# Performance work log

Measured on AMD Instinct MI355X. Metric: run time of the kernel, lower is better.

## Reference

```python
import jax, jax.numpy as jnp
import numpy as np

C_IMG = 16
GRID = 128
NV = 100000
NE = 1600000
CH = (32, 64, 64)
SCALE = 0.1
STEPS = 1
SLOPE = 0.3  # LeakyReLU default in module


def setup_inputs() -> dict:
    key = jax.random.key(0)
    ks = jax.random.split(key, 20)
    image_features = jax.random.normal(ks[0], (C_IMG, GRID, GRID, GRID), jnp.float32)
    # vertices live in voxel coordinates of the feature grid
    vertices = jax.random.uniform(ks[1], (NV, 3), jnp.float32) * (GRID - 1)
    edge_src = jax.random.randint(ks[2], (NE,), 0, NV, jnp.int32)
    edge_dst = jax.random.randint(ks[3], (NE,), 0, NV, jnp.int32)
    dims = [C_IMG + 3] + list(CH) + [3]  # +3 normalized positions
    inp = {"image_features": image_features, "vertices": vertices,
           "edge_src": edge_src, "edge_dst": edge_dst}
    ki = 4
    for i in range(len(dims) - 1):
        fan_in = dims[i]
        s = 1.0 / np.sqrt(fan_in)
        inp[f"w_self{i}"] = jax.random.normal(ks[ki], (dims[i], dims[i + 1]), jnp.float32) * s
        inp[f"w_nb{i}"] = jax.random.normal(ks[ki + 1], (dims[i], dims[i + 1]), jnp.float32) * s
        inp[f"b{i}"] = jnp.zeros((dims[i + 1],), jnp.float32)
        ki += 2
    return inp


def trilinear_sample(img, verts):
    # img: (C, W, H, D); verts: (V, 3) voxel coords -> (V, C)
    C, W, H, D = img.shape
    hi = jnp.array([W - 1, H - 1, D - 1], verts.dtype)
    p = jnp.clip(verts, 0.0, hi)
    p0 = jnp.floor(p)
    i0 = p0.astype(jnp.int32)
    i1 = jnp.minimum(i0 + 1, hi.astype(jnp.int32))
    w = p - p0
    x0, y0, z0 = i0[:, 0], i0[:, 1], i0[:, 2]
    x1, y1, z1 = i1[:, 0], i1[:, 1], i1[:, 2]
    wx, wy, wz = w[:, 0:1], w[:, 1:2], w[:, 2:3]

    def g(xi, yi, zi):
        return img[:, xi, yi, zi].T  # (V, C)

    c00 = g(x0, y0, z0) * (1 - wz) + g(x0, y0, z1) * wz
    c01 = g(x0, y1, z0) * (1 - wz) + g(x0, y1, z1) * wz
    c10 = g(x1, y0, z0) * (1 - wz) + g(x1, y0, z1) * wz
    c11 = g(x1, y1, z0) * (1 - wz) + g(x1, y1, z1) * wz
    return (c00 * (1 - wy) + c01 * wy) * (1 - wx) + (c10 * (1 - wy) + c11 * wy) * wx


def edge_conv(x, src, dst, inv_deg, w_self, w_nb, b):
    nb = jax.ops.segment_sum(x[src], dst, num_segments=x.shape[0]) * inv_deg
    return x @ w_self + nb @ w_nb + b


def reference(image_features, vertices, edge_src, edge_dst,
              w_self0, w_nb0, b0, w_self1, w_nb1, b1,
              w_self2, w_nb2, b2, w_self3, w_nb3, b3):
    nv = vertices.shape[0]
    deg = jax.ops.segment_sum(jnp.ones((edge_src.shape[0],), jnp.float32), edge_dst,
                              num_segments=nv)
    inv_deg = (1.0 / jnp.maximum(deg, 1.0))[:, None]
    grid_max = jnp.float32(max(image_features.shape[1:]))  # image_shape.max()
    layers = [(w_self0, w_nb0, b0), (w_self1, w_nb1, b1), (w_self2, w_nb2, b2)]
    for _ in range(STEPS):
        feats = trilinear_sample(image_features, vertices)
        feats = jnp.concatenate([vertices / grid_max, feats], axis=-1)
        h = feats
        for (ws, wn, b) in layers:
            h = jax.nn.leaky_relu(edge_conv(h, edge_src, edge_dst, inv_deg, ws, wn, b), SLOPE)
        deformation = edge_conv(h, edge_src, edge_dst, inv_deg, w_self3, w_nb3, b3)
        vertices = vertices + SCALE * deformation
    return vertices
```

## Files before the change

### kernel.cpp

```cpp
#include <hip/hip_runtime.h>

#define C_IMG 16
#define GRIDSZ 128
#define VOL (GRIDSZ * GRIDSZ * GRIDSZ)
#define SLOPE 0.3f
#define SCALE 0.1f
#define EPB 4096
#define CAPB 12288
#define BIN_CAP 16384

#define BT0_OFF 0
#define BT1_OFF 2048
#define BT2_OFF 6144
#define BT_TOTAL 14336

using f4_t  = __attribute__((ext_vector_type(4))) float;
using bf8_t = __attribute__((ext_vector_type(8))) short;

__device__ __forceinline__ unsigned int bf16_pack2(float a, float b) {
    unsigned int ua = __float_as_uint(a);
    ua = (ua + 0x7FFFu + ((ua >> 16) & 1u)) >> 16;
    unsigned int ub = __float_as_uint(b);
    ub = (ub + 0x7FFFu + ((ub >> 16) & 1u)) >> 16;
    return ua | (ub << 16);
}
__device__ __forceinline__ unsigned short bf16_1(float a) {
    unsigned int ua = __float_as_uint(a);
    return (unsigned short)((ua + 0x7FFFu + ((ua >> 16) & 1u)) >> 16);
}
__device__ __forceinline__ float bf_lo(unsigned int u) { return __uint_as_float(u << 16); }
__device__ __forceinline__ float bf_hi(unsigned int u) { return __uint_as_float(u & 0xFFFF0000u); }

__global__ __launch_bounds__(256) void k_prepw(const float* __restrict__ ws0,
                                               const float* __restrict__ wn0,
                                               const float* __restrict__ ws1,
                                               const float* __restrict__ wn1,
                                               const float* __restrict__ ws2,
                                               const float* __restrict__ wn2,
                                               unsigned short* __restrict__ btab) {
    int i = blockIdx.x * 256 + threadIdx.x;
    if (i < 2048) {
        int c = i >> 6, kk = i & 63;
        int j = (kk < 32) ? kk : kk - 32;
        const float* W = (kk < 32) ? ws0 : wn0;
        float w = 0.f;
        if (j < 19) { int sr = (j < 16) ? (j + 3) : (j - 16); w = W[sr * 32 + c]; }
        btab[BT0_OFF + c * 64 + kk] = bf16_1(w);
    } else if (i < 6144) {
        int t = i - 2048;
        int c = t >> 6, kk = t & 63;
        int j = (kk < 32) ? kk : kk - 32;
        const float* W = (kk < 32) ? ws1 : wn1;
        btab[BT1_OFF + c * 64 + kk] = bf16_1(W[j * 64 + c]);
    } else if (i < BT_TOTAL) {
        int t = i - 6144;
        int c = t >> 7, kk = t & 127;
        int j = (kk < 64) ? kk : kk - 64;
        const float* W = (kk < 64) ? ws2 : wn2;
        btab[BT2_OFF + c * 128 + kk] = bf16_1(W[j * 64 + c]);
    }
}

__global__ __launch_bounds__(256) void k_transpose(const float* __restrict__ img,
                                                   unsigned int* __restrict__ timg) {
    const int tid = threadIdx.x;
    const int xy = blockIdx.x;
    const int zlo = tid & 31;
    const int half = (tid >> 5) & 1;
    const int zhi = tid >> 6;
    const int z = zhi * 32 + zlo;
    const size_t ib = (size_t)xy * GRIDSZ + z;
    const int c0 = half * 8;
    float f[8];
    #pragma unroll
    for (int c = 0; c < 8; ++c)
        f[c] = img[(size_t)(c0 + c) * VOL + ib];
    uint4 o;
    o.x = bf16_pack2(f[0], f[1]);
    o.y = bf16_pack2(f[2], f[3]);
    o.z = bf16_pack2(f[4], f[5]);
    o.w = bf16_pack2(f[6], f[7]);
    *(uint4*)(timg + ((size_t)xy * GRIDSZ + z) * 8 + half * 4) = o;
}

__global__ __launch_bounds__(256) void k_bucket(const int* __restrict__ esrc,
                                                const int* __restrict__ edst,
                                                int* __restrict__ bucketCursor,
                                                unsigned int* __restrict__ pairs,
                                                int* __restrict__ rowStart,
                                                int ne, int nv) {
    __shared__ unsigned int hist[256];
    __shared__ unsigned int pref[256];
    __shared__ unsigned int curs[256];
    __shared__ unsigned int gbase[256];
    __shared__ unsigned int stage_v[EPB];
    __shared__ unsigned char stage_b[EPB];
    const int tid = threadIdx.x;
    const int base = blockIdx.x * EPB;
    const int n = min(EPB, ne - base);
    if (blockIdx.x == 0 && tid == 0) rowStart[nv] = ne;
    hist[tid] = 0;
    __syncthreads();
    for (int i = tid; i < n; i += 256)
        atomicAdd(&hist[((unsigned)edst[base + i]) >> 9], 1u);
    __syncthreads();
    const unsigned int h = hist[tid];
    pref[tid] = h;
    __syncthreads();
    #pragma unroll
    for (int off = 1; off < 256; off <<= 1) {
        unsigned int t = (tid >= off) ? pref[tid - off] : 0;
        __syncthreads();
        pref[tid] += t;
        __syncthreads();
    }
    const unsigned int excl = pref[tid] - h;
    if (h) {
        int pos = atomicAdd(&bucketCursor[tid], (int)h);
        if (pos > CAPB - (int)h) pos = CAPB - (int)h;
        gbase[tid] = (unsigned int)(tid * CAPB + pos);
    } else {
        gbase[tid] = 0u;
    }
    __syncthreads();
    pref[tid] = excl;
    curs[tid] = excl;
    __syncthreads();
    for (int i = tid; i < n; i += 256) {
        unsigned int d = (unsigned)edst[base + i];
        unsigned int s = (unsigned)esrc[base + i];
        unsigned int p = atomicAdd(&curs[d >> 9], 1u);
        stage_v[p] = (s << 9) | (d & 511u);
        stage_b[p] = (unsigned char)(d >> 9);
    }
    __syncthreads();
    for (int i = tid; i < n; i += 256) {
        unsigned int b = stage_b[i];
        pairs[gbase[b] + (unsigned)i - pref[b]] = stage_v[i];
    }
}

__global__ __launch_bounds__(256) void k_binsort(const unsigned int* __restrict__ pairs,
                                                 const int* __restrict__ bucketCursor,
                                                 int* __restrict__ rowStart,
                                                 float* __restrict__ invdeg,
                                                 int* __restrict__ csrSrc, int nv) {
    __shared__ int deg_s[512];
    __shared__ int rs_s[512];
    __shared__ int cur_s[512];
    __shared__ int scan_s[256];
    __shared__ int bb[256];
    __shared__ int outbuf[BIN_CAP];
    const int tid = threadIdx.x;
    const int b = blockIdx.x;
    const int vbase = b << 9;
    if (vbase >= nv) return;
    const int nvb = min(512, nv - vbase);
    const int c = min(bucketCursor[tid], CAPB);
    bb[tid] = c;
    deg_s[tid] = 0;
    deg_s[tid + 256] = 0;
    __syncthreads();
    #pragma unroll
    for (int off = 1; off < 256; off <<= 1) {
        int t = (tid >= off) ? bb[tid - off] : 0;
        __syncthreads();
        bb[tid] += t;
        __syncthreads();
    }
    const int count = min(bucketCursor[b], CAPB);
    const int gs = bb[b] - count;
    const unsigned int* pbase = pairs + (size_t)b * CAPB;
    for (int i = tid; i < count; i += 256) {
        unsigned int p = pbase[i];
        atomicAdd(&deg_s[p & 511u], 1);
    }
    __syncthreads();
    const int d0 = deg_s[2 * tid];
    const int d1 = deg_s[2 * tid + 1];
    const int ps = d0 + d1;
    scan_s[tid] = ps;
    __syncthreads();
    #pragma unroll
    for (int off = 1; off < 256; off <<= 1) {
        int t = (tid >= off) ? scan_s[tid - off] : 0;
        __syncthreads();
        scan_s[tid] += t;
        __syncthreads();
    }
    const int epair = scan_s[tid] - ps;
    rs_s[2 * tid] = epair;
    rs_s[2 * tid + 1] = epair + d0;
    cur_s[2 * tid] = epair;
    cur_s[2 * tid + 1] = epair + d0;
    #pragma unroll
    for (int u = 0; u < 2; ++u) {
        int idx = 2 * tid + u;
        if (idx < nvb) {
            rowStart[vbase + idx] = gs + rs_s[idx];
            int d = deg_s[idx];
            invdeg[vbase + idx] = 1.0f / (float)(d > 1 ? d : 1);
        }
    }
    __syncthreads();
    for (int i = tid; i < count; i += 256) {
        unsigned int p = pbase[i];
        int pos = atomicAdd(&cur_s[p & 511u], 1);
        outbuf[pos] = (int)(p >> 9);
    }
    __syncthreads();
    for (int i = tid; i < count; i += 256) csrSrc[gs + i] = outbuf[i];
}

__global__ __launch_bounds__(256) void k_sample(const unsigned int* __restrict__ timg,
                                                const float* __restrict__ verts,
                                                unsigned int* __restrict__ feats, int nv) {
    int t = blockIdx.x * 256 + threadIdx.x;
    int v = t >> 1;
    int q = t & 1;
    if (v >= nv) return;
    float px = verts[v * 3 + 0];
    float py = verts[v * 3 + 1];
    float pz = verts[v * 3 + 2];
    float cx = fminf(fmaxf(px, 0.0f), 127.0f);
    float cy = fminf(fmaxf(py, 0.0f), 127.0f);
    float cz = fminf(fmaxf(pz, 0.0f), 127.0f);
    float fx = floorf(cx), fy = floorf(cy), fz = floorf(cz);
    int x0 = (int)fx, y0 = (int)fy, z0 = (int)fz;
    int x1 = min(x0 + 1, 127), y1 = min(y0 + 1, 127), z1 = min(z0 + 1, 127);
    float wx = cx - fx, wy = cy - fy, wz = cz - fz;
    const int qo = q * 4;
    #define LD(X, Y, Z) (*(const uint4*)(timg + ((size_t)((((X) << 7) + (Y)) << 7) + (size_t)(Z)) * 8 + qo))
    uint4 f000 = LD(x0, y0, z0), f001 = LD(x0, y0, z1);
    uint4 f010 = LD(x0, y1, z0), f011 = LD(x0, y1, z1);
    uint4 f100 = LD(x1, y0, z0), f101 = LD(x1, y0, z1);
    uint4 f110 = LD(x1, y1, z0), f111 = LD(x1, y1, z1);
    #undef LD
    float r[8];
    const unsigned int* a000 = (const unsigned int*)&f000;
    const unsigned int* a001 = (const unsigned int*)&f001;
    const unsigned int* a010 = (const unsigned int*)&f010;
    const unsigned int* a011 = (const unsigned int*)&f011;
    const unsigned int* a100 = (const unsigned int*)&f100;
    const unsigned int* a101 = (const unsigned int*)&f101;
    const unsigned int* a110 = (const unsigned int*)&f110;
    const unsigned int* a111 = (const unsigned int*)&f111;
    #pragma unroll
    for (int u = 0; u < 4; ++u) {
        float c00l = bf_lo(a000[u]) * (1.f - wz) + bf_lo(a001[u]) * wz;
        float c01l = bf_lo(a010[u]) * (1.f - wz) + bf_lo(a011[u]) * wz;
        float c10l = bf_lo(a100[u]) * (1.f - wz) + bf_lo(a101[u]) * wz;
        float c11l = bf_lo(a110[u]) * (1.f - wz) + bf_lo(a111[u]) * wz;
        r[2 * u] = (c00l * (1.f - wy) + c01l * wy) * (1.f - wx) +
                   (c10l * (1.f - wy) + c11l * wy) * wx;
        float c00h = bf_hi(a000[u]) * (1.f - wz) + bf_hi(a001[u]) * wz;
        float c01h = bf_hi(a010[u]) * (1.f - wz) + bf_hi(a011[u]) * wz;
        float c10h = bf_hi(a100[u]) * (1.f - wz) + bf_hi(a101[u]) * wz;
        float c11h = bf_hi(a110[u]) * (1.f - wz) + bf_hi(a111[u]) * wz;
        r[2 * u + 1] = (c00h * (1.f - wy) + c01h * wy) * (1.f - wx) +
                       (c10h * (1.f - wy) + c11h * wy) * wx;
    }
    unsigned int* row = feats + (size_t)v * 16;
    uint4 o;
    o.x = bf16_pack2(r[0], r[1]); o.y = bf16_pack2(r[2], r[3]);
    o.z = bf16_pack2(r[4], r[5]); o.w = bf16_pack2(r[6], r[7]);
    *(uint4*)(row + q * 4) = o;
    if (q == 0) {
        uint4 o2;
        o2.x = bf16_pack2(px * (1.0f / 128.0f), py * (1.0f / 128.0f));
        o2.y = bf16_pack2(pz * (1.0f / 128.0f), 0.0f);
        o2.z = 0u; o2.w = 0u;
        *(uint4*)(row + 8) = o2;
        *(uint4*)(row + 12) = make_uint4(0u, 0u, 0u, 0u);
    }
}

template <int KX, int COUT, bool PREMUL>
__global__ __launch_bounds__(256) void k_layer_fused(const unsigned int* __restrict__ x,
                                                     const unsigned short* __restrict__ btab,
                                                     const int* __restrict__ rowStart,
                                                     const int* __restrict__ csrSrc,
                                                     const float* __restrict__ invdeg,
                                                     const float* __restrict__ bias,
                                                     unsigned int* __restrict__ out, int nv,
                                                     const float* __restrict__ Wn3,
                                                     unsigned int* __restrict__ zout) {
    constexpr int KTOT = 2 * KX;
    constexpr int NT = COUT / 16;
    constexpr int MT = 2;
    constexpr int SXU = KX / 2;
    constexpr int KS = KX / 32;
    constexpr int VPB = 128;
    constexpr int NCH = KX / 8;
    constexpr int NBW = KX + 8;
    __shared__ __align__(16) unsigned short nb_s[VPB * NBW];

    const int vb0 = blockIdx.x * VPB;
    for (int task = threadIdx.x; task < VPB * NCH; task += 256) {
        const int vloc = task / NCH;
        const int ch = task - vloc * NCH;
        const int v = vb0 + vloc;
        unsigned short* dst = nb_s + vloc * NBW + ch * 8;
        if (v < nv) {
            int beg = rowStart[v];
            int end = rowStart[v + 1];
            float a0 = 0.f, a1 = 0.f, a2 = 0.f, a3 = 0.f,
                  a4 = 0.f, a5 = 0.f, a6 = 0.f, a7 = 0.f;
            int j = beg;
            for (; j + 3 < end; j += 4) {
                int s0 = csrSrc[j];
                int s1 = csrSrc[j + 1];
                int s2 = csrSrc[j + 2];
                int s3 = csrSrc[j + 3];
                uint4 q0 = ((const uint4*)(x + (size_t)s0 * SXU))[ch];
                uint4 q1 = ((const uint4*)(x + (size_t)s1 * SXU))[ch];
                uint4 q2 = ((const uint4*)(x + (size_t)s2 * SXU))[ch];
                uint4 q3 = ((const uint4*)(x + (size_t)s3 * SXU))[ch];
                a0 += bf_lo(q0.x); a1 += bf_hi(q0.x);
                a2 += bf_lo(q0.y); a3 += bf_hi(q0.y);
                a4 += bf_lo(q0.z); a5 += bf_hi(q0.z);
                a6 += bf_lo(q0.w); a7 += bf_hi(q0.w);
                a0 += bf_lo(q1.x); a1 += bf_hi(q1.x);
                a2 += bf_lo(q1.y); a3 += bf_hi(q1.y);
                a4 += bf_lo(q1.z); a5 += bf_hi(q1.z);
                a6 += bf_lo(q1.w); a7 += bf_hi(q1.w);
                a0 += bf_lo(q2.x); a1 += bf_hi(q2.x);
                a2 += bf_lo(q2.y); a3 += bf_hi(q2.y);
                a4 += bf_lo(q2.z); a5 += bf_hi(q2.z);
                a6 += bf_lo(q2.w); a7 += bf_hi(q2.w);
                a0 += bf_lo(q3.x); a1 += bf_hi(q3.x);
                a2 += bf_lo(q3.y); a3 += bf_hi(q3.y);
                a4 += bf_lo(q3.z); a5 += bf_hi(q3.z);
                a6 += bf_lo(q3.w); a7 += bf_hi(q3.w);
            }
            for (; j < end; ++j) {
                int s = csrSrc[j];
                uint4 q = ((const uint4*)(x + (size_t)s * SXU))[ch];
                a0 += bf_lo(q.x); a1 += bf_hi(q.x);
                a2 += bf_lo(q.y); a3 += bf_hi(q.y);
                a4 += bf_lo(q.z); a5 += bf_hi(q.z);
                a6 += bf_lo(q.w); a7 += bf_hi(q.w);
            }
            const float id = invdeg[v];
            uint4 o;
            o.x = bf16_pack2(a0 * id, a1 * id); o.y = bf16_pack2(a2 * id, a3 * id);
            o.z = bf16_pack2(a4 * id, a5 * id); o.w = bf16_pack2(a6 * id, a7 * id);
            *(uint4*)dst = o;
        } else {
            *(uint4*)dst = make_uint4(0u, 0u, 0u, 0u);
        }
    }
    __syncthreads();

    const int lane = threadIdx.x & 63;
    const int wid = threadIdx.x >> 6;
    const int v0 = vb0 + wid * (MT * 16);
    const int row = lane & 15;
    const int kg = lane >> 4;

    f4_t acc[MT][NT] = {};

    #pragma unroll
    for (int ks = 0; ks < 2 * KS; ++ks) {
        bf8_t afrag[MT];
        if (ks < KS) {
            const int kbase = ks * 32;
            #pragma unroll
            for (int mt = 0; mt < MT; ++mt) {
                int v = v0 + mt * 16 + row;
                v = min(v, nv - 1);
                afrag[mt] = *(const bf8_t*)(x + (size_t)v * SXU + ((kbase + kg * 8) >> 1));
            }
        } else {
            const int kbase = (ks - KS) * 32;
            #pragma unroll
            for (int mt = 0; mt < MT; ++mt) {
                const int vloc = wid * (MT * 16) + mt * 16 + row;
                afrag[mt] = *(const bf8_t*)(nb_s + vloc * NBW + kbase + kg * 8);
            }
        }
        #pragma unroll
        for (int nt = 0; nt < NT; ++nt) {
            bf8_t bfrag = *(const bf8_t*)(btab + (nt * 16 + row) * KTOT + ks * 32 + kg * 8);
            #pragma unroll
            for (int mt = 0; mt < MT; ++mt)
                acc[mt][nt] = __builtin_amdgcn_mfma_f32_16x16x32_bf16(afrag[mt], bfrag,
                                                                      acc[mt][nt], 0, 0, 0);
        }
    }

    unsigned short* po = (unsigned short*)out;
    float bq[NT];
    #pragma unroll
    for (int nt = 0; nt < NT; ++nt) bq[nt] = bias[nt * 16 + row];
    float wz[PREMUL ? NT : 1][3];
    if constexpr (PREMUL) {
        #pragma unroll
        for (int nt = 0; nt < NT; ++nt) {
            const float* wr = Wn3 + (nt * 16 + row) * 3;
            wz[nt][0] = wr[0]; wz[nt][1] = wr[1]; wz[nt][2] = wr[2];
        }
    }
    #pragma unroll
    for (int mt = 0; mt < MT; ++mt) {
        #pragma unroll
        for (int r = 0; r < 4; ++r) {
            const int v = v0 + mt * 16 + kg * 4 + r;
            float tv[NT];
            #pragma unroll
            for (int nt = 0; nt < NT; ++nt) {
                float t = acc[mt][nt][r] + bq[nt];
                t = (t >= 0.f) ? t : SLOPE * t;
                tv[nt] = t;
                if (v < nv) po[(size_t)v * COUT + nt * 16 + row] = bf16_1(t);
            }
            if constexpr (PREMUL) {
                float z0 = 0.f, z1 = 0.f, z2 = 0.f;
                #pragma unroll
                for (int nt = 0; nt < NT; ++nt) {
                    z0 += tv[nt] * wz[nt][0];
                    z1 += tv[nt] * wz[nt][1];
                    z2 += tv[nt] * wz[nt][2];
                }
                #pragma unroll
                for (int m = 1; m < 16; m <<= 1) {
                    z0 += __shfl_xor(z0, m);
                    z1 += __shfl_xor(z1, m);
                    z2 += __shfl_xor(z2, m);
                }
                if (row == 0 && v < nv) {
                    uint2 o;
                    o.x = bf16_pack2(z0, z1);
                    o.y = bf16_pack2(z2, 0.f);
                    *(uint2*)(zout + (size_t)v * 2) = o;
                }
            }
        }
    }
}

__global__ __launch_bounds__(256) void k_final(const unsigned int* __restrict__ h,
                                               const unsigned int* __restrict__ z,
                                               const int* __restrict__ rowStart,
                                               const int* __restrict__ csrSrc,
                                               const float* __restrict__ invdeg,
                                               const float* __restrict__ ws,
                                               const float* __restrict__ b,
                                               const float* __restrict__ verts,
                                               float* __restrict__ out, int nv) {
    __shared__ float w_s[64 * 3];
    if (threadIdx.x < 64 * 3) w_s[threadIdx.x] = ws[threadIdx.x];
    __syncthreads();
    int v = blockIdx.x * 256 + threadIdx.x;
    if (v >= nv) return;
    float n0 = 0.f, n1 = 0.f, n2 = 0.f;
    {
        int beg = rowStart[v];
        int end = rowStart[v + 1];
        int j = beg;
        for (; j + 3 < end; j += 4) {
            int s0 = csrSrc[j];
            int s1 = csrSrc[j + 1];
            int s2 = csrSrc[j + 2];
            int s3 = csrSrc[j + 3];
            uint2 q0 = *(const uint2*)(z + (size_t)s0 * 2);
            uint2 q1 = *(const uint2*)(z + (size_t)s1 * 2);
            uint2 q2 = *(const uint2*)(z + (size_t)s2 * 2);
            uint2 q3 = *(const uint2*)(z + (size_t)s3 * 2);
            n0 += bf_lo(q0.x); n1 += bf_hi(q0.x); n2 += bf_lo(q0.y);
            n0 += bf_lo(q1.x); n1 += bf_hi(q1.x); n2 += bf_lo(q1.y);
            n0 += bf_lo(q2.x); n1 += bf_hi(q2.x); n2 += bf_lo(q2.y);
            n0 += bf_lo(q3.x); n1 += bf_hi(q3.x); n2 += bf_lo(q3.y);
        }
        for (; j < end; ++j) {
            int s = csrSrc[j];
            uint2 q = *(const uint2*)(z + (size_t)s * 2);
            n0 += bf_lo(q.x); n1 += bf_hi(q.x); n2 += bf_lo(q.y);
        }
    }
    const uint4* hr = (const uint4*)(h + (size_t)v * 32);
    float a0 = b[0], a1 = b[1], a2 = b[2];
    #pragma unroll
    for (int q = 0; q < 8; ++q) {
        uint4 hv = hr[q];
        float f[8] = {bf_lo(hv.x), bf_hi(hv.x), bf_lo(hv.y), bf_hi(hv.y),
                      bf_lo(hv.z), bf_hi(hv.z), bf_lo(hv.w), bf_hi(hv.w)};
        #pragma unroll
        for (int i = 0; i < 8; ++i) {
            int k = q * 8 + i;
            a0 += f[i] * w_s[k * 3 + 0];
            a1 += f[i] * w_s[k * 3 + 1];
            a2 += f[i] * w_s[k * 3 + 2];
        }
    }
    float id = invdeg[v];
    a0 += n0 * id; a1 += n1 * id; a2 += n2 * id;
    out[(size_t)v * 3 + 0] = verts[(size_t)v * 3 + 0] + SCALE * a0;
    out[(size_t)v * 3 + 1] = verts[(size_t)v * 3 + 1] + SCALE * a1;
    out[(size_t)v * 3 + 2] = verts[(size_t)v * 3 + 2] + SCALE * a2;
}

extern "C" void kernel_launch(void* const* d_in, const int* in_sizes, int n_in,
                              void* d_out, int out_size, void* d_ws, size_t ws_size,
                              hipStream_t stream) {
    const float* img   = (const float*)d_in[0];
    const float* verts = (const float*)d_in[1];
    const int*   esrc  = (const int*)d_in[2];
    const int*   edst  = (const int*)d_in[3];
    const float* ws0 = (const float*)d_in[4];
    const float* wn0 = (const float*)d_in[5];
    const float* b0  = (const float*)d_in[6];
    const float* ws1 = (const float*)d_in[7];
    const float* wn1 = (const float*)d_in[8];
    const float* b1  = (const float*)d_in[9];
    const float* ws2 = (const float*)d_in[10];
    const float* wn2 = (const float*)d_in[11];
    const float* b2  = (const float*)d_in[12];
    const float* ws3 = (const float*)d_in[13];
    const float* wn3 = (const float*)d_in[14];
    const float* b3  = (const float*)d_in[15];

    const int nv = in_sizes[1] / 3;
    const int ne = in_sizes[2];

    char* base = (char*)d_ws;
    size_t off = 0;
    auto alloc = [&](size_t bytes) -> void* {
        off = (off + 255) & ~(size_t)255;
        void* p = base + off;
        off += bytes;
        return p;
    };
    float* invdeg   = (float*)alloc((size_t)nv * 4);
    int*   rowStart = (int*)alloc((size_t)(nv + 1) * 4);
    int*   bucketCursor = (int*)alloc(256 * 4);
    int*   csrSrc   = (int*)alloc((size_t)ne * 4);
    unsigned int* pairs = (unsigned int*)alloc((size_t)256 * CAPB * 4);
    unsigned int* A   = (unsigned int*)alloc((size_t)nv * 32 * 4);
    unsigned int* B   = (unsigned int*)alloc((size_t)nv * 32 * 4);
    unsigned int* Z   = (unsigned int*)alloc((size_t)nv * 2 * 4);
    unsigned short* btab = (unsigned short*)alloc(BT_TOTAL * 2);
    unsigned int* timg = (unsigned int*)alloc((size_t)VOL * 16 * 2);

    auto blocks = [](long long n) { return (int)((n + 255) / 256); };
    const int nbuckets = (nv + 511) >> 9;
    const int lb = (nv + 127) / 128;

    hipMemsetAsync(bucketCursor, 0, 256 * 4, stream);
    k_prepw<<<(BT_TOTAL + 255) / 256, 256, 0, stream>>>(ws0, wn0, ws1, wn1, ws2, wn2, btab);
    k_transpose<<<GRIDSZ * GRIDSZ, 256, 0, stream>>>(img, timg);
    k_bucket<<<(ne + EPB - 1) / EPB, 256, 0, stream>>>(esrc, edst, bucketCursor,
                                                       pairs, rowStart, ne, nv);
    k_binsort<<<nbuckets, 256, 0, stream>>>(pairs, bucketCursor, rowStart, invdeg, csrSrc, nv);

    k_sample<<<blocks((long long)nv * 2), 256, 0, stream>>>(timg, verts, A, nv);

    k_layer_fused<32, 32, false><<<lb, 256, 0, stream>>>(
        A, btab + BT0_OFF, rowStart, csrSrc, invdeg, b0, B, nv, nullptr, nullptr);

    k_layer_fused<32, 64, false><<<lb, 256, 0, stream>>>(
        B, btab + BT1_OFF, rowStart, csrSrc, invdeg, b1, A, nv, nullptr, nullptr);

    k_layer_fused<64, 64, true><<<lb, 256, 0, stream>>>(
        A, btab + BT2_OFF, rowStart, csrSrc, invdeg, b2, B, nv, wn3, Z);

    k_final<<<blocks(nv), 256, 0, stream>>>(
        B, Z, rowStart, csrSrc, invdeg, ws3, b3, verts, (float*)d_out, nv);
}
```

Measured before the change: 416.4 us.

## Merge preprocessing kernels into one launch and degree-sort vertices in gather

Weight prep, image transpose and edge bucketing now run as one kernel whose blocks branch on block index, removing two launches and letting these independent stages overlap. In the layer kernels, per-vertex row bounds are cached in shared memory, and vertices are ranked by degree so that neighbour-gather tasks in the same wavefront have similar loop lengths, reducing divergence. The trade-offs are that the fused kernel reserves the bucketing kernel's shared memory for every block, which can lower occupancy for the transpose blocks, and that the O(128) rank loop adds work at the start of each layer block.

```diff
diff --git a/kernel.cpp b/kernel.cpp
--- a/kernel.cpp
+++ b/kernel.cpp
@@ -13,6 +13,7 @@
 #define BT1_OFF 2048
 #define BT2_OFF 6144
 #define BT_TOTAL 14336
+#define PREPW_BLOCKS ((BT_TOTAL + 255) / 256)
 
 using f4_t  = __attribute__((ext_vector_type(4))) float;
 using bf8_t = __attribute__((ext_vector_type(8))) short;
@@ -31,64 +32,21 @@
 __device__ __forceinline__ float bf_lo(unsigned int u) { return __uint_as_float(u << 16); }
 __device__ __forceinline__ float bf_hi(unsigned int u) { return __uint_as_float(u & 0xFFFF0000u); }
 
-__global__ __launch_bounds__(256) void k_prepw(const float* __restrict__ ws0,
-                                               const float* __restrict__ wn0,
-                                               const float* __restrict__ ws1,
-                                               const float* __restrict__ wn1,
-                                               const float* __restrict__ ws2,
-                                               const float* __restrict__ wn2,
-                                               unsigned short* __restrict__ btab) {
-    int i = blockIdx.x * 256 + threadIdx.x;
-    if (i < 2048) {
-        int c = i >> 6, kk = i & 63;
-        int j = (kk < 32) ? kk : kk - 32;
-        const float* W = (kk < 32) ? ws0 : wn0;
-        float w = 0.f;
-        if (j < 19) { int sr = (j < 16) ? (j + 3) : (j - 16); w = W[sr * 32 + c]; }
-        btab[BT0_OFF + c * 64 + kk] = bf16_1(w);
-    } else if (i < 6144) {
-        int t = i - 2048;
-        int c = t >> 6, kk = t & 63;
-        int j = (kk < 32) ? kk : kk - 32;
-        const float* W = (kk < 32) ? ws1 : wn1;
-        btab[BT1_OFF + c * 64 + kk] = bf16_1(W[j * 64 + c]);
-    } else if (i < BT_TOTAL) {
-        int t = i - 6144;
-        int c = t >> 7, kk = t & 127;
-        int j = (kk < 64) ? kk : kk - 64;
-        const float* W = (kk < 64) ? ws2 : wn2;
-        btab[BT2_OFF + c * 128 + kk] = bf16_1(W[j * 64 + c]);
-    }
-}
-
-__global__ __launch_bounds__(256) void k_transpose(const float* __restrict__ img,
-                                                   unsigned int* __restrict__ timg) {
-    const int tid = threadIdx.x;
-    const int xy = blockIdx.x;
-    const int zlo = tid & 31;
-    const int half = (tid >> 5) & 1;
-    const int zhi = tid >> 6;
-    const int z = zhi * 32 + zlo;
-    const size_t ib = (size_t)xy * GRIDSZ + z;
-    const int c0 = half * 8;
-    float f[8];
-    #pragma unroll
-    for (int c = 0; c < 8; ++c)
-        f[c] = img[(size_t)(c0 + c) * VOL + ib];
-    uint4 o;
-    o.x = bf16_pack2(f[0], f[1]);
-    o.y = bf16_pack2(f[2], f[3]);
-    o.z = bf16_pack2(f[4], f[5]);
-    o.w = bf16_pack2(f[6], f[7]);
-    *(uint4*)(timg + ((size_t)xy * GRIDSZ + z) * 8 + half * 4) = o;
-}
-
-__global__ __launch_bounds__(256) void k_bucket(const int* __restrict__ esrc,
-                                                const int* __restrict__ edst,
-                                                int* __restrict__ bucketCursor,
-                                                unsigned int* __restrict__ pairs,
-                                                int* __restrict__ rowStart,
-                                                int ne, int nv) {
+__global__ __launch_bounds__(256) void k_pre(const float* __restrict__ img,
+                                             unsigned int* __restrict__ timg,
+                                             const float* __restrict__ ws0,
+                                             const float* __restrict__ wn0,
+                                             const float* __restrict__ ws1,
+                                             const float* __restrict__ wn1,
+                                             const float* __restrict__ ws2,
+                                             const float* __restrict__ wn2,
+                                             unsigned short* __restrict__ btab,
+                                             const int* __restrict__ esrc,
+                                             const int* __restrict__ edst,
+                                             int* __restrict__ bucketCursor,
+                                             unsigned int* __restrict__ pairs,
+                                             int* __restrict__ rowStart,
+                                             int ne, int nv, int nbb) {
     __shared__ unsigned int hist[256];
     __shared__ unsigned int pref[256];
     __shared__ unsigned int curs[256];
@@ -96,47 +54,90 @@
     __shared__ unsigned int stage_v[EPB];
     __shared__ unsigned char stage_b[EPB];
     const int tid = threadIdx.x;
-    const int base = blockIdx.x * EPB;
-    const int n = min(EPB, ne - base);
-    if (blockIdx.x == 0 && tid == 0) rowStart[nv] = ne;
-    hist[tid] = 0;
-    __syncthreads();
-    for (int i = tid; i < n; i += 256)
-        atomicAdd(&hist[((unsigned)edst[base + i]) >> 9], 1u);
-    __syncthreads();
-    const unsigned int h = hist[tid];
-    pref[tid] = h;
-    __syncthreads();
-    #pragma unroll
-    for (int off = 1; off < 256; off <<= 1) {
-        unsigned int t = (tid >= off) ? pref[tid - off] : 0;
-        __syncthreads();
-        pref[tid] += t;
-        __syncthreads();
-    }
-    const unsigned int excl = pref[tid] - h;
-    if (h) {
-        int pos = atomicAdd(&bucketCursor[tid], (int)h);
-        if (pos > CAPB - (int)h) pos = CAPB - (int)h;
-        gbase[tid] = (unsigned int)(tid * CAPB + pos);
+
+    if (blockIdx.x < (unsigned)nbb) {
+        const int base = blockIdx.x * EPB;
+        const int n = min(EPB, ne - base);
+        if (blockIdx.x == 0 && tid == 0) rowStart[nv] = ne;
+        hist[tid] = 0;
+        __syncthreads();
+        for (int i = tid; i < n; i += 256)
+            atomicAdd(&hist[((unsigned)edst[base + i]) >> 9], 1u);
+        __syncthreads();
+        const unsigned int h = hist[tid];
+        pref[tid] = h;
+        __syncthreads();
+        #pragma unroll
+        for (int off = 1; off < 256; off <<= 1) {
+            unsigned int t = (tid >= off) ? pref[tid - off] : 0;
+            __syncthreads();
+            pref[tid] += t;
+            __syncthreads();
+        }
+        const unsigned int excl = pref[tid] - h;
+        if (h) {
+            int pos = atomicAdd(&bucketCursor[tid], (int)h);
+            if (pos > CAPB - (int)h) pos = CAPB - (int)h;
+            gbase[tid] = (unsigned int)(tid * CAPB + pos);
+        } else {
+            gbase[tid] = 0u;
+        }
+        __syncthreads();
+        pref[tid] = excl;
+        curs[tid] = excl;
+        __syncthreads();
+        for (int i = tid; i < n; i += 256) {
+            unsigned int d = (unsigned)edst[base + i];
+            unsigned int s = (unsigned)esrc[base + i];
+            unsigned int p = atomicAdd(&curs[d >> 9], 1u);
+            stage_v[p] = (s << 9) | (d & 511u);
+            stage_b[p] = (unsigned char)(d >> 9);
+        }
+        __syncthreads();
+        for (int i = tid; i < n; i += 256) {
+            unsigned int b = stage_b[i];
+            pairs[gbase[b] + (unsigned)i - pref[b]] = stage_v[i];
+        }
+    } else if (blockIdx.x < (unsigned)(nbb + PREPW_BLOCKS)) {
+        int i = (blockIdx.x - nbb) * 256 + tid;
+        if (i < 2048) {
+            int c = i >> 6, kk = i & 63;
+            int j = (kk < 32) ? kk : kk - 32;
+            const float* W = (kk < 32) ? ws0 : wn0;
+            float w = 0.f;
+            if (j < 19) { int sr = (j < 16) ? (j + 3) : (j - 16); w = W[sr * 32 + c]; }
+            btab[BT0_OFF + c * 64 + kk] = bf16_1(w);
+        } else if (i < 6144) {
+            int t = i - 2048;
+            int c = t >> 6, kk = t & 63;
+            int j = (kk < 32) ? kk : kk - 32;
+            const float* W = (kk < 32) ? ws1 : wn1;
+            btab[BT1_OFF + c * 64 + kk] = bf16_1(W[j * 64 + c]);
+        } else if (i < BT_TOTAL) {
+            int t = i - 6144;
+            int c = t >> 7, kk = t & 127;
+            int j = (kk < 64) ? kk : kk - 64;
+            const float* W = (kk < 64) ? ws2 : wn2;
+            btab[BT2_OFF + c * 128 + kk] = bf16_1(W[j * 64 + c]);
+        }
     } else {
-        gbase[tid] = 0u;
-    }
-    __syncthreads();
-    pref[tid] = excl;
-    curs[tid] = excl;
-    __syncthreads();
-    for (int i = tid; i < n; i += 256) {
-        unsigned int d = (unsigned)edst[base + i];
-        unsigned int s = (unsigned)esrc[base + i];
-        unsigned int p = atomicAdd(&curs[d >> 9], 1u);
-        stage_v[p] = (s << 9) | (d & 511u);
-        stage_b[p] = (unsigned char)(d >> 9);
-    }
-    __syncthreads();
-    for (int i = tid; i < n; i += 256) {
-        unsigned int b = stage_b[i];
-        pairs[gbase[b] + (unsigned)i - pref[b]] = stage_v[i];
+        const int xy = blockIdx.x - nbb - PREPW_BLOCKS;
+        const int zlo = tid & 31;
+        const int half = (tid >> 5) & 1;
+        const int zhi = tid >> 6;
+        const int z = zhi * 32 + zlo;
+        const size_t ib = (size_t)xy * GRIDSZ + z;
+        const int c0 = half * 8;
+        float f[8];
+        #pragma unroll
+        for (int c = 0; c < 8; ++c)
+            f[c] = img[(size_t)(c0 + c) * VOL + ib];
+        uint4 o;
+        o.x = bf16_pack2(f[0], f[1]);
+        o.y = bf16_pack2(f[2], f[3]);
+        o.z = bf16_pack2(f[4], f[5]);
+        o.w = bf16_pack2(f[6], f[7]);
+        *(uint4*)(timg + ((size_t)xy * GRIDSZ + z) * 8 + half * 4) = o;
     }
 }
 
@@ -292,18 +293,45 @@
     constexpr int KS = KX / 32;
     constexpr int VPB = 128;
     constexpr int NCH = KX / 8;
+    constexpr int LOG_NCH = (KX == 32) ? 2 : 3;
     constexpr int NBW = KX + 8;
     __shared__ __align__(16) unsigned short nb_s[VPB * NBW];
+    __shared__ int beg_s[VPB];
+    __shared__ int end_s[VPB];
+    __shared__ unsigned short order_s[VPB];
 
     const int vb0 = blockIdx.x * VPB;
-    for (int task = threadIdx.x; task < VPB * NCH; task += 256) {
-        const int vloc = task / NCH;
-        const int ch = task - vloc * NCH;
+    const int tid = threadIdx.x;
+
+    if (tid < VPB) {
+        int v = vb0 + tid;
+        int b = 0, e = 0;
+        if (v < nv) { b = rowStart[v]; e = rowStart[v + 1]; }
+        beg_s[tid] = b;
+        end_s[tid] = e;
+    }
+    __syncthreads();
+    if (tid < VPB) {
+        const int d = end_s[tid] - beg_s[tid];
+        int rank = 0;
+        #pragma unroll 4
+        for (int j = 0; j < VPB; ++j) {
+            int dj = end_s[j] - beg_s[j];
+            rank += (dj < d) || (dj == d && j < tid);
+        }
+        order_s[rank] = (unsigned short)tid;
+    }
+    __syncthreads();
+
+    for (int task = tid; task < VPB * NCH; task += 256) {
+        const int srt = task >> LOG_NCH;
+        const int ch = task & (NCH - 1);
+        const int vloc = order_s[srt];
         const int v = vb0 + vloc;
         unsigned short* dst = nb_s + vloc * NBW + ch * 8;
         if (v < nv) {
-            int beg = rowStart[v];
-            int end = rowStart[v + 1];
+            const int beg = beg_s[vloc];
+            const int end = end_s[vloc];
             float a0 = 0.f, a1 = 0.f, a2 = 0.f, a3 = 0.f,
                   a4 = 0.f, a5 = 0.f, a6 = 0.f, a7 = 0.f;
             int j = beg;
@@ -352,8 +380,8 @@
     }
     __syncthreads();
 
-    const int lane = threadIdx.x & 63;
-    const int wid = threadIdx.x >> 6;
+    const int lane = tid & 63;
+    const int wid = tid >> 6;
     const int v0 = vb0 + wid * (MT * 16);
     const int row = lane & 15;
     const int kg = lane >> 4;
@@ -544,13 +572,13 @@
 
     auto blocks = [](long long n) { return (int)((n + 255) / 256); };
     const int nbuckets = (nv + 511) >> 9;
+    const int nbb = (ne + EPB - 1) / EPB;
     const int lb = (nv + 127) / 128;
 
     hipMemsetAsync(bucketCursor, 0, 256 * 4, stream);
-    k_prepw<<<(BT_TOTAL + 255) / 256, 256, 0, stream>>>(ws0, wn0, ws1, wn1, ws2, wn2, btab);
-    k_transpose<<<GRIDSZ * GRIDSZ, 256, 0, stream>>>(img, timg);
-    k_bucket<<<(ne + EPB - 1) / EPB, 256, 0, stream>>>(esrc, edst, bucketCursor,
-                                                       pairs, rowStart, ne, nv);
+    k_pre<<<nbb + PREPW_BLOCKS + GRIDSZ * GRIDSZ, 256, 0, stream>>>(
+        img, timg, ws0, wn0, ws1, wn1, ws2, wn2, btab,
+        esrc, edst, bucketCursor, pairs, rowStart, ne, nv, nbb);
     k_binsort<<<nbuckets, 256, 0, stream>>>(pairs, bucketCursor, rowStart, invdeg, csrSrc, nv);
 
     k_sample<<<blocks((long long)nv * 2), 256, 0, stream>>>(timg, verts, A, nv);
```

Result: faster. 400.6 us (-3.8%).
